# Kernel tuning notes

Hardware: AMD Instinct MI355X
Metric: run time of the kernel (lower is better)

Reference implementation:

```python
import jax, jax.numpy as jnp
import numpy as np

WS = (2, 7, 7)   # window size (d, h, w)
NH = 4           # num heads
EPS = 1e-5       # LayerNorm eps (torch default)


def _rel_index():
    wd, wh, ww = WS
    coords = np.stack(np.meshgrid(np.arange(wd), np.arange(wh), np.arange(ww), indexing='ij'))  # (3,wd,wh,ww)
    cf = coords.reshape(3, -1)                      # (3, N)
    rel = cf[:, :, None] - cf[:, None, :]           # (3, N, N)
    rel = rel.transpose(1, 2, 0).astype(np.int64)   # (N, N, 3)
    rel[..., 0] += wd - 1
    rel[..., 1] += wh - 1
    rel[..., 2] += ww - 1
    rel[..., 0] *= (2 * wh - 1) * (2 * ww - 1)
    rel[..., 1] *= (2 * ww - 1)
    return jnp.asarray(rel.sum(-1), dtype=jnp.int32)  # (N, N)


def setup_inputs() -> dict:
    key = jax.random.key(0)
    ks = jax.random.split(key, 6)
    C, CH = 128, 512
    TBL = (2 * WS[0] - 1) * (2 * WS[1] - 1) * (2 * WS[2] - 1)  # 507
    rn = lambda k, s, sc=0.02: jax.random.normal(k, s, jnp.float32) * sc
    return {
        'x': jax.random.normal(ks[0], (2, 8, 56, 56, C), jnp.float32),
        'norm1_w': jnp.ones((C,), jnp.float32), 'norm1_b': jnp.zeros((C,), jnp.float32),
        'qkv_w': rn(ks[1], (3 * C, C)), 'qkv_b': jnp.zeros((3 * C,), jnp.float32),
        'bias_table': rn(ks[2], (TBL, NH)),
        'proj_w': rn(ks[3], (C, C)), 'proj_b': jnp.zeros((C,), jnp.float32),
        'norm2_w': jnp.ones((C,), jnp.float32), 'norm2_b': jnp.zeros((C,), jnp.float32),
        'fc1_w': rn(ks[4], (CH, C)), 'fc1_b': jnp.zeros((CH,), jnp.float32),
        'fc2_w': rn(ks[5], (C, CH)), 'fc2_b': jnp.zeros((C,), jnp.float32),
        'rel_index': _rel_index(),
    }


def _layernorm(x, w, b):
    m = jnp.mean(x, axis=-1, keepdims=True)
    v = jnp.mean(jnp.square(x - m), axis=-1, keepdims=True)
    return (x - m) * jax.lax.rsqrt(v + EPS) * w + b


def reference(x, norm1_w, norm1_b, qkv_w, qkv_b, bias_table, proj_w, proj_b,
              norm2_w, norm2_b, fc1_w, fc1_b, fc2_w, fc2_b, rel_index):
    B, D, H, W, C = x.shape
    wd, wh, ww = WS
    N = wd * wh * ww
    hd = C // NH

    shortcut = x
    xn = _layernorm(x, norm1_w, norm1_b)
    # window partition: (B,D,H,W,C) -> (B*nW, N, C)
    xw = xn.reshape(B, D // wd, wd, H // wh, wh, W // ww, ww, C)
    xw = xw.transpose(0, 1, 3, 5, 2, 4, 6, 7).reshape(-1, N, C)
    B_ = xw.shape[0]

    qkv = (xw @ qkv_w.T + qkv_b).reshape(B_, N, 3, NH, hd).transpose(2, 0, 3, 1, 4)
    q, k, v = qkv[0] * (hd ** -0.5), qkv[1], qkv[2]   # (B_, NH, N, hd)
    attn = jnp.einsum('bhnd,bhmd->bhnm', q, k)
    bias = bias_table[rel_index.reshape(-1)].reshape(N, N, NH).transpose(2, 0, 1)  # (NH,N,N)
    attn = jax.nn.softmax(attn + bias[None], axis=-1)
    out = jnp.einsum('bhnm,bhmd->bhnd', attn, v).transpose(0, 2, 1, 3).reshape(B_, N, C)
    out = out @ proj_w.T + proj_b

    # window reverse: (B*nW, N, C) -> (B,D,H,W,C)
    xr = out.reshape(B, D // wd, H // wh, W // ww, wd, wh, ww, C)
    xr = xr.transpose(0, 1, 4, 2, 5, 3, 6, 7).reshape(B, D, H, W, C)

    x = shortcut + xr
    h = _layernorm(x, norm2_w, norm2_b)
    h = jax.nn.gelu(h @ fc1_w.T + fc1_b, approximate=False)  # torch nn.GELU = exact erf
    return x + (h @ fc2_w.T + fc2_b)
```

## Files before the change

### kernel.cpp

```cpp
#include <hip/hip_runtime.h>
#include <hip/hip_bf16.h>

typedef __hip_bfloat16 bf16;
typedef unsigned short u16t;
typedef unsigned int u32t;
typedef __attribute__((ext_vector_type(8))) short bf16x8_t;
typedef __attribute__((ext_vector_type(4))) float f32x4_t;

#define DEVI static __device__ __forceinline__

DEVI float u2f(u32t bits) { union { u32t u; float f; } v; v.u = bits; return v.f; }
DEVI float bflo(u32t u) { return u2f((u & 0xffffu) << 16); }
DEVI float bfhi(u32t u) { return u2f(u & 0xffff0000u); }
DEVI float sh2f(short s) { return u2f(((u32t)(u16t)s) << 16); }
DEVI float bf2f(bf16 h) { return __bfloat162float(h); }
DEVI bf16 f2bf(float f) { return __float2bfloat16(f); }
DEVI u16t f2bfbits(float f) {
  bf16 h = __float2bfloat16(f);
  union { bf16 h; u16t u; } v; v.h = h; return v.u;
}

DEVI void gl_lds16(const void* g, void* l) {
  __builtin_amdgcn_global_load_lds(
      (const __attribute__((address_space(1))) unsigned int*)g,
      (__attribute__((address_space(3))) unsigned int*)l, 16, 0, 0);
}

#define TOK   50176
#define NWIN  512
#define NTOK  98
#define NHEAD 4
#define HDIM  32
#define QSCALE 0.17677669529663687f

__global__ __launch_bounds__(256) void setup_k(
    const float* __restrict__ a, const float* __restrict__ b,
    const float* __restrict__ c, const float* __restrict__ d,
    bf16* __restrict__ o,
    const float* __restrict__ btab, const int* __restrict__ relidx,
    const float* __restrict__ qkv_b, float* __restrict__ BmatT,
    float* __restrict__ bsc) {
  int bx = blockIdx.x;
  if (bx < 768) {
    int i = bx * 256 + threadIdx.x;
    const float* s; int off;
    if (i < 49152)       { s = a; off = 0; }
    else if (i < 65536)  { s = b; off = 49152; }
    else if (i < 131072) { s = c; off = 65536; }
    else                 { s = d; off = 131072; }
    float v = s[i - off];
    if (i < 16384) v *= QSCALE;
    o[i] = f2bf(v);
  } else {
    int idx = (bx - 768) * 256 + threadIdx.x;
    if (idx < NTOK * NTOK) {
      int i = idx / NTOK, j = idx - i * NTOK;
      int r = relidx[idx] * NHEAD;
#pragma unroll
      for (int h = 0; h < NHEAD; h++)
        BmatT[(size_t)(h * NTOK + j) * 112 + i] = btab[r + h];
    }
    if (bx == 768 && threadIdx.x < 384)
      bsc[threadIdx.x] = qkv_b[threadIdx.x] * (threadIdx.x < 128 ? QSCALE : 1.0f);
  }
}

DEVI int winrev(int grow) {
  int nw = grow / NTOK, n = grow - nw * NTOK;
  int wq = nw & 7, hq = (nw >> 3) & 7, dq = (nw >> 6) & 3, bb = nw >> 8;
  int wr = n % 7; int q7 = n / 7; int hr = q7 % 7, dr = q7 / 7;
  return ((bb * 8 + dq * 2 + dr) * 56 + hq * 7 + hr) * 56 + wq * 7 + wr;
}

__global__ __launch_bounds__(512, 4) void qkvln_k(
    const float* __restrict__ x, const float* __restrict__ n1w,
    const float* __restrict__ n1b, const bf16* __restrict__ W,
    const float* __restrict__ bsc, bf16* __restrict__ qkvO)
{
  __shared__ __align__(16) short As[128 * 128];
  __shared__ __align__(16) short Bs[128 * 128];
  const int tid = threadIdx.x;
  const int rowBase = blockIdx.x << 7;
  const int wv = tid >> 6, lane = tid & 63;
  const int q = lane >> 4, r16 = lane & 15;

#pragma unroll
  for (int t = 0; t < 4; t++) {
    int f = tid + (t << 9);
    int row = f >> 4, cs = (f & 15) ^ (row & 15);
    gl_lds16((const u16t*)W + (size_t)row * 128 + (cs << 3), &Bs[f << 3]);
  }

  {
    const int c = lane << 1;
    float lw0 = n1w[c], lw1 = n1w[c + 1];
    float lb0 = n1b[c], lb1 = n1b[c + 1];
#pragma unroll
    for (int rr = 0; rr < 16; rr++) {
      int row = (wv << 4) + rr;
      int tt = winrev(rowBase + row);
      float2 xv = *(const float2*)(x + (size_t)tt * 128 + c);
      float x0 = xv.x, x1 = xv.y;
      float s = x0 + x1, ss = x0 * x0 + x1 * x1;
#pragma unroll
      for (int m = 32; m; m >>= 1) { s += __shfl_xor(s, m); ss += __shfl_xor(ss, m); }
      float mean = s * 0.0078125f;
      float var = ss * 0.0078125f - mean * mean;
      float rstd = rsqrtf(var + 1e-5f);
      float y0 = (x0 - mean) * rstd * lw0 + lb0;
      float y1 = (x1 - mean) * rstd * lw1 + lb1;
      u32t ov = ((u32t)f2bfbits(y1) << 16) | (u32t)f2bfbits(y0);
      int slot = (lane >> 2) ^ (row & 15);
      *(u32t*)&As[(row << 7) + (slot << 3) + ((lane & 3) << 1)] = ov;
    }
  }
  __syncthreads();

#pragma unroll 1
  for (int qt = 0; qt < 3; qt++) {
    if (qt > 0) {
#pragma unroll
      for (int t = 0; t < 4; t++) {
        int f = tid + (t << 9);
        int row = f >> 4, cs = (f & 15) ^ (row & 15);
        gl_lds16((const u16t*)W + (size_t)((qt << 7) + row) * 128 + (cs << 3),
                 &Bs[f << 3]);
      }
      __syncthreads();
    }
    f32x4_t acc[8];
#pragma unroll
    for (int j = 0; j < 8; j++) acc[j] = (f32x4_t){0.f, 0.f, 0.f, 0.f};
#pragma unroll
    for (int ks = 0; ks < 4; ks++) {
      int rowA = (wv << 4) + r16;
      int slotA = ((ks << 2) + q) ^ (rowA & 15);
      bf16x8_t af = *(const bf16x8_t*)&As[(rowA << 7) + (slotA << 3)];
      bf16x8_t bfr[8];
#pragma unroll
      for (int nt = 0; nt < 8; nt++) {
        int row = (nt << 4) + r16;
        int slot = ((ks << 2) + q) ^ (row & 15);
        bfr[nt] = *(const bf16x8_t*)&Bs[(row << 7) + (slot << 3)];
      }
#pragma unroll
      for (int nt = 0; nt < 8; nt++)
        acc[nt] = __builtin_amdgcn_mfma_f32_16x16x32_bf16(af, bfr[nt], acc[nt], 0, 0, 0);
    }
    float bv[8];
#pragma unroll
    for (int nt = 0; nt < 8; nt++) bv[nt] = bsc[(qt << 7) + (nt << 4) + r16];
    __syncthreads();
#pragma unroll
    for (int reg = 0; reg < 4; reg++) {
      int lrow = (wv << 4) + (q << 2) + reg;
#pragma unroll
      for (int nt = 0; nt < 8; nt++)
        Bs[(lrow << 7) + (nt << 4) + r16] = (short)f2bfbits(acc[nt][reg] + bv[nt]);
    }
    __syncthreads();
#pragma unroll
    for (int t = 0; t < 4; t++) {
      int f = tid + (t << 9);
      int row = f >> 4, c8 = (f & 15) << 3;
      size_t ob = (size_t)(rowBase + row) * 384 + (qt << 7) + c8;
      *(uint4*)((u16t*)qkvO + ob) = *(const uint4*)&Bs[(row << 7) + c8];
    }
    if (qt < 2) __syncthreads();
  }
}

__global__ __launch_bounds__(512, 4) void proj_k(
    const bf16* __restrict__ A, const bf16* __restrict__ W,
    const float* __restrict__ bias, const float* __restrict__ resX,
    bf16* __restrict__ outB, bf16* __restrict__ outB2,
    const float* __restrict__ lnw, const float* __restrict__ lnb)
{
  __shared__ __align__(16) short As[128 * 128];
  __shared__ __align__(16) short Bs[128 * 128];
  const int tid = threadIdx.x;
  const int rowBase = blockIdx.x << 7;
  const int wv = tid >> 6, lane = tid & 63;
  const int q = lane >> 4, r16 = lane & 15;
  const int mB = wv << 4;

#pragma unroll
  for (int t = 0; t < 4; t++) {
    int f = tid + (t << 9);
    int row = f >> 4, cs = (f & 15) ^ (row & 15);
    gl_lds16((const u16t*)A + (size_t)(rowBase + row) * 128 + (cs << 3),
             &As[f << 3]);
  }
#pragma unroll
  for (int t = 0; t < 4; t++) {
    int f = tid + (t << 9);
    int row = f >> 4, cs = (f & 15) ^ (row & 15);
    gl_lds16((const u16t*)W + (size_t)row * 128 + (cs << 3), &Bs[f << 3]);
  }
  __syncthreads();

  f32x4_t acc[8];
#pragma unroll
  for (int j = 0; j < 8; j++) acc[j] = (f32x4_t){0.f, 0.f, 0.f, 0.f};
#pragma unroll
  for (int ks = 0; ks < 4; ks++) {
    int rowA = mB + r16;
    int slotA = ((ks << 2) + q) ^ (rowA & 15);
    bf16x8_t af = *(const bf16x8_t*)&As[(rowA << 7) + (slotA << 3)];
    bf16x8_t bfr[8];
#pragma unroll
    for (int nt = 0; nt < 8; nt++) {
      int row = (nt << 4) + r16;
      int slot = ((ks << 2) + q) ^ (row & 15);
      bfr[nt] = *(const bf16x8_t*)&Bs[(row << 7) + (slot << 3)];
    }
#pragma unroll
    for (int nt = 0; nt < 8; nt++)
      acc[nt] = __builtin_amdgcn_mfma_f32_16x16x32_bf16(af, bfr[nt], acc[nt], 0, 0, 0);
  }
  __syncthreads();

  float bv[8];
#pragma unroll
  for (int nt = 0; nt < 8; nt++) bv[nt] = bias[(nt << 4) + r16];

#pragma unroll
  for (int reg = 0; reg < 4; reg++) {
    int lrow = mB + (q << 2) + reg;
#pragma unroll
    for (int nt = 0; nt < 8; nt++)
      As[(lrow << 7) + (nt << 4) + r16] = (short)f2bfbits(acc[nt][reg] + bv[nt]);
  }
  __syncthreads();
#pragma unroll
  for (int t = 0; t < 4; t++) {
    int f = tid + (t << 9);
    int row = f >> 4, c8 = (f & 15) << 3;
    int tt = winrev(rowBase + row);
    size_t ob = (size_t)tt * 128 + c8;
    float4 r0 = *(const float4*)(resX + ob);
    float4 r1 = *(const float4*)(resX + ob + 4);
    short* cs = &As[(row << 7) + c8];
    u16t pk[8];
    pk[0] = f2bfbits(sh2f(cs[0]) + r0.x); pk[1] = f2bfbits(sh2f(cs[1]) + r0.y);
    pk[2] = f2bfbits(sh2f(cs[2]) + r0.z); pk[3] = f2bfbits(sh2f(cs[3]) + r0.w);
    pk[4] = f2bfbits(sh2f(cs[4]) + r1.x); pk[5] = f2bfbits(sh2f(cs[5]) + r1.y);
    pk[6] = f2bfbits(sh2f(cs[6]) + r1.z); pk[7] = f2bfbits(sh2f(cs[7]) + r1.w);
    *(uint4*)((u16t*)outB + ob) = *(const uint4*)pk;
    *(uint4*)cs = *(const uint4*)pk;
  }
  __syncthreads();
  const int c = lane << 1;
  float2 lw = *(const float2*)(lnw + c);
  float2 lb = *(const float2*)(lnb + c);
#pragma unroll 4
  for (int rr = 0; rr < 16; rr++) {
    int row = (wv << 4) + rr;
    u32t u = *(const u32t*)&As[(row << 7) + c];
    float x0 = bflo(u), x1 = bfhi(u);
    float s = x0 + x1, ss = x0 * x0 + x1 * x1;
#pragma unroll
    for (int m = 32; m; m >>= 1) { s += __shfl_xor(s, m); ss += __shfl_xor(ss, m); }
    float mean = s * 0.0078125f;
    float var = ss * 0.0078125f - mean * mean;
    float rstd = rsqrtf(var + 1e-5f);
    float y0 = (x0 - mean) * rstd * lw.x + lb.x;
    float y1 = (x1 - mean) * rstd * lw.y + lb.y;
    int tt = winrev(rowBase + row);
    u32t ov = ((u32t)f2bfbits(y1) << 16) | (u32t)f2bfbits(y0);
    *(u32t*)((u16t*)outB2 + (size_t)tt * 128 + c) = ov;
  }
}

__global__ __launch_bounds__(512, 4) void mlp_fused_k(
    const bf16* __restrict__ Axn, const bf16* __restrict__ F1,
    const bf16* __restrict__ F2, const float* __restrict__ b1,
    const float* __restrict__ b2, const bf16* __restrict__ resB,
    float* __restrict__ out)
{
  __shared__ __align__(16) char smem[81920];
  short* As  = (short*)smem;
  short* F1s = (short*)(smem + 32768);
  short* F2s = (short*)(smem + 49152);
  short* Hs  = (short*)(smem + 65536);
  float* Cf  = (float*)smem;

  const int tid = threadIdx.x;
  const int rowBase = blockIdx.x << 7;
  const int wv = tid >> 6, lane = tid & 63;
  const int q = lane >> 4, r16 = lane & 15;
  const int mB = wv << 4;

#pragma unroll
  for (int t = 0; t < 4; t++) {
    int f = tid + (t << 9);
    int row = f >> 4, cs = (f & 15) ^ (row & 15);
    gl_lds16((const u16t*)Axn + (size_t)(rowBase + row) * 128 + (cs << 3),
             &As[f << 3]);
  }
#pragma unroll
  for (int t = 0; t < 2; t++) {
    int f = tid + (t << 9);
    int row = f >> 4, cs = (f & 15) ^ (row & 15);
    gl_lds16((const u16t*)F1 + (size_t)row * 128 + (cs << 3), &F1s[f << 3]);
  }
#pragma unroll
  for (int t = 0; t < 2; t++) {
    int f = tid + (t << 9);
    int row = f >> 3, cs = (f & 7) ^ (row & 7);
    gl_lds16((const u16t*)F2 + (size_t)row * 512 + (cs << 3), &F2s[f << 3]);
  }
  __syncthreads();

  f32x4_t oacc[8];
#pragma unroll
  for (int j = 0; j < 8; j++) oacc[j] = (f32x4_t){0.f, 0.f, 0.f, 0.f};

#pragma unroll 1
  for (int c = 0; c < 8; c++) {
    if (c > 0) {
#pragma unroll
      for (int t = 0; t < 2; t++) {
        int f = tid + (t << 9);
        int row = f >> 4, cs = (f & 15) ^ (row & 15);
        gl_lds16((const u16t*)F1 + (size_t)(c * 64 + row) * 128 + (cs << 3),
                 &F1s[f << 3]);
      }
#pragma unroll
      for (int t = 0; t < 2; t++) {
        int f = tid + (t << 9);
        int row = f >> 3, cs = (f & 7) ^ (row & 7);
        gl_lds16((const u16t*)F2 + (size_t)row * 512 + c * 64 + (cs << 3),
                 &F2s[f << 3]);
      }
      __syncthreads();
    }

    f32x4_t hacc[4];
#pragma unroll
    for (int j = 0; j < 4; j++) hacc[j] = (f32x4_t){0.f, 0.f, 0.f, 0.f};
#pragma unroll
    for (int ks = 0; ks < 4; ks++) {
      int rowA = mB + r16;
      int slotA = ((ks << 2) + q) ^ (rowA & 15);
      bf16x8_t af = *(const bf16x8_t*)&As[(rowA << 7) + (slotA << 3)];
      bf16x8_t bfr[4];
#pragma unroll
      for (int nt = 0; nt < 4; nt++) {
        int row = (nt << 4) + r16;
        int slot = ((ks << 2) + q) ^ (row & 15);
        bfr[nt] = *(const bf16x8_t*)&F1s[(row << 7) + (slot << 3)];
      }
#pragma unroll
      for (int nt = 0; nt < 4; nt++)
        hacc[nt] = __builtin_amdgcn_mfma_f32_16x16x32_bf16(af, bfr[nt], hacc[nt], 0, 0, 0);
    }

    float bb[4];
#pragma unroll
    for (int nt = 0; nt < 4; nt++) bb[nt] = b1[c * 64 + (nt << 4) + r16];
#pragma unroll
    for (int reg = 0; reg < 4; reg++) {
      int lrow = mB + (q << 2) + reg;
#pragma unroll
      for (int nt = 0; nt < 4; nt++) {
        float v = hacc[nt][reg] + bb[nt];
        v = 0.5f * v * (1.0f + erff(v * 0.70710678118654752f));
        int col = (nt << 4) + r16;
        int sp = (col >> 3) ^ (lrow & 7);
        Hs[(lrow << 6) + (sp << 3) + (col & 7)] = (short)f2bfbits(v);
      }
    }
    __syncthreads();

#pragma unroll
    for (int ks = 0; ks < 2; ks++) {
      int rowA = mB + r16;
      int slotA = ((ks << 2) + q) ^ (rowA & 7);
      bf16x8_t af = *(const bf16x8_t*)&Hs[(rowA << 6) + (slotA << 3)];
      bf16x8_t bfr[8];
#pragma unroll
      for (int nt = 0; nt < 8; nt++) {
        int row = (nt << 4) + r16;
        int slot = ((ks << 2) + q) ^ (row & 7);
        bfr[nt] = *(const bf16x8_t*)&F2s[(row << 6) + (slot << 3)];
      }
#pragma unroll
      for (int nt = 0; nt < 8; nt++)
        oacc[nt] = __builtin_amdgcn_mfma_f32_16x16x32_bf16(af, bfr[nt], oacc[nt], 0, 0, 0);
    }
    __syncthreads();
  }

  float bv[8];
#pragma unroll
  for (int nt = 0; nt < 8; nt++) bv[nt] = b2[(nt << 4) + r16];
#pragma unroll
  for (int reg = 0; reg < 4; reg++) {
    int lrow = mB + (q << 2) + reg;
#pragma unroll
    for (int nt = 0; nt < 8; nt++)
      Cf[lrow * 132 + (nt << 4) + r16] = oacc[nt][reg] + bv[nt];
  }
  __syncthreads();
#pragma unroll
  for (int t = 0; t < 8; t++) {
    int f = tid + (t << 9);
    int row = f >> 5, c4 = (f & 31) << 2;
    size_t ob = (size_t)(rowBase + row) * 128 + c4;
    const u16t* rp = (const u16t*)resB + ob;
    const float* cp = &Cf[row * 132 + c4];
    float4 v;
    v.x = cp[0] + sh2f(rp[0]);
    v.y = cp[1] + sh2f(rp[1]);
    v.z = cp[2] + sh2f(rp[2]);
    v.w = cp[3] + sh2f(rp[3]);
    *(float4*)(out + ob) = v;
  }
}

#define PSTR 136
__global__ __launch_bounds__(256) void attn_mfma_k(
    const bf16* __restrict__ qkv, const float* __restrict__ BmatT,
    bf16* __restrict__ out)
{
  __shared__ short Vt[32 * PSTR];
  __shared__ short Ps[112 * PSTR];
  const int nw = blockIdx.x, h = blockIdx.y;
  const int tid = threadIdx.x;
  const int wv = tid >> 6, lane = tid & 63;
  const int q = lane >> 4, r16 = lane & 15;

  for (int idx = tid; idx < 32 * 38; idx += 256) {
    int d = idx / 38, j = 98 + idx % 38;
    Vt[d * PSTR + j] = 0;
  }
  for (int idx = tid; idx < 112 * 12; idx += 256) {
    int r = idx / 12, c = (idx % 12) << 1;
    *(u32t*)&Ps[r * PSTR + 112 + c] = 0;
  }
  for (int idx = tid; idx < NTOK * 16; idx += 256) {
    int j = idx >> 4, d2 = (idx & 15) << 1;
    u32t uv = *(const u32t*)((const u16t*)qkv +
                             (size_t)(nw * NTOK + j) * 384 + 256 + h * 32 + d2);
    Vt[d2 * PSTR + j] = (short)(uv & 0xffffu);
    Vt[(d2 + 1) * PSTR + j] = (short)(uv >> 16);
  }

  const int mt0 = wv;
  const bool has2 = (wv + 4) < 7;
  const int mt1 = has2 ? wv + 4 : wv;

  int i0 = mt0 * 16 + r16; if (i0 > NTOK - 1) i0 = NTOK - 1;
  int i1 = mt1 * 16 + r16; if (i1 > NTOK - 1) i1 = NTOK - 1;
  bf16x8_t aq0 = *(const bf16x8_t*)((const u16t*)qkv +
      (size_t)(nw * NTOK + i0) * 384 + h * 32 + (q << 3));
  bf16x8_t aq1 = *(const bf16x8_t*)((const u16t*)qkv +
      (size_t)(nw * NTOK + i1) * 384 + h * 32 + (q << 3));

  f32x4_t sc[2][7];
#pragma unroll
  for (int nt = 0; nt < 7; nt++) {
    int j = (nt << 4) + r16; if (j > NTOK - 1) j = NTOK - 1;
    const float* bRow = &BmatT[(size_t)(h * NTOK + j) * 112];
    bf16x8_t bk = *(const bf16x8_t*)((const u16t*)qkv +
        (size_t)(nw * NTOK + j) * 384 + 128 + h * 32 + (q << 3));
    f32x4_t b0 = *(const f32x4_t*)&bRow[mt0 * 16 + (q << 2)];
    f32x4_t b1 = *(const f32x4_t*)&bRow[mt1 * 16 + (q << 2)];
    sc[0][nt] = __builtin_amdgcn_mfma_f32_16x16x32_bf16(aq0, bk, b0, 0, 0, 0);
    sc[1][nt] = __builtin_amdgcn_mfma_f32_16x16x32_bf16(aq1, bk, b1, 0, 0, 0);
  }

#pragma unroll
  for (int sel = 0; sel < 2; sel++) {
    if (sel == 1 && !has2) break;
    int mtile = sel ? mt1 : mt0;
    int ibase = mtile * 16 + (q << 2);
    float s[4][7];
#pragma unroll
    for (int nt = 0; nt < 7; nt++) {
      int j = (nt << 4) + r16;
#pragma unroll
      for (int reg = 0; reg < 4; reg++) {
        int i = ibase + reg;
        s[reg][nt] = (i < NTOK && j < NTOK) ? sc[sel][nt][reg] : -1.0e30f;
      }
    }
#pragma unroll
    for (int reg = 0; reg < 4; reg++) {
      float m = -3.0e38f;
#pragma unroll
      for (int nt = 0; nt < 7; nt++) m = fmaxf(m, s[reg][nt]);
#pragma unroll
      for (int d = 8; d; d >>= 1) m = fmaxf(m, __shfl_xor(m, d));
      float sum = 0.f;
#pragma unroll
      for (int nt = 0; nt < 7; nt++) { s[reg][nt] = __expf(s[reg][nt] - m); sum += s[reg][nt]; }
#pragma unroll
      for (int d = 8; d; d >>= 1) sum += __shfl_xor(sum, d);
      float inv = 1.f / sum;
#pragma unroll
      for (int nt = 0; nt < 7; nt++)
        Ps[(ibase + reg) * PSTR + (nt << 4) + r16] =
            (short)f2bfbits(s[reg][nt] * inv);
    }
  }

  __syncthreads();

#pragma unroll
  for (int sel = 0; sel < 2; sel++) {
    if (sel == 1 && !has2) break;
    int mtile = sel ? mt1 : mt0;
    f32x4_t o0 = {0.f, 0.f, 0.f, 0.f}, o1 = {0.f, 0.f, 0.f, 0.f};
#pragma unroll
    for (int kt = 0; kt < 4; kt++) {
      bf16x8_t ap = *(const bf16x8_t*)&Ps[(mtile * 16 + r16) * PSTR + (kt << 5) + (q << 3)];
      bf16x8_t bv0 = *(const bf16x8_t*)&Vt[r16 * PSTR + (kt << 5) + (q << 3)];
      bf16x8_t bv1 = *(const bf16x8_t*)&Vt[(16 + r16) * PSTR + (kt << 5) + (q << 3)];
      o0 = __builtin_amdgcn_mfma_f32_16x16x32_bf16(ap, bv0, o0, 0, 0, 0);
      o1 = __builtin_amdgcn_mfma_f32_16x16x32_bf16(ap, bv1, o1, 0, 0, 0);
    }
#pragma unroll
    for (int reg = 0; reg < 4; reg++) {
      int i = mtile * 16 + (q << 2) + reg;
      if (i < NTOK) {
        size_t ob = (size_t)(nw * NTOK + i) * 128 + h * 32;
        out[ob + r16] = f2bf(o0[reg]);
        out[ob + 16 + r16] = f2bf(o1[reg]);
      }
    }
  }
}

extern "C" void kernel_launch(void* const* d_in, const int* in_sizes, int n_in,
                              void* d_out, int out_size, void* d_ws, size_t ws_size,
                              hipStream_t stream) {
  const float* x      = (const float*)d_in[0];
  const float* n1w    = (const float*)d_in[1];
  const float* n1b    = (const float*)d_in[2];
  const float* qkv_w  = (const float*)d_in[3];
  const float* qkv_b  = (const float*)d_in[4];
  const float* btab   = (const float*)d_in[5];
  const float* proj_w = (const float*)d_in[6];
  const float* proj_b = (const float*)d_in[7];
  const float* n2w    = (const float*)d_in[8];
  const float* n2b    = (const float*)d_in[9];
  const float* fc1_w  = (const float*)d_in[10];
  const float* fc1_b  = (const float*)d_in[11];
  const float* fc2_w  = (const float*)d_in[12];
  const float* fc2_b  = (const float*)d_in[13];
  const int*   relidx = (const int*)d_in[14];

  const size_t Asz = (size_t)TOK * 128 * 2;
  char* ws = (char*)d_ws;
  bf16* wbf   = (bf16*)ws;
  bf16* qkvw16  = wbf;
  bf16* projw16 = wbf + 49152;
  bf16* fc1w16  = wbf + 65536;
  bf16* fc2w16  = wbf + 131072;
  float* BmatT = (float*)(ws + 393216);
  float* bsc   = (float*)(ws + 393216 + 175616);
  char* R = ws + (1 << 20);
  bf16* attn  = (bf16*)d_out;
  bf16* qkv   = (bf16*)R;
  bf16* x2    = (bf16*)R;
  bf16* xn2   = (bf16*)(R + Asz);
  float* out  = (float*)d_out;

  setup_k<<<806, 256, 0, stream>>>(qkv_w, proj_w, fc1_w, fc2_w, wbf,
                                   btab, relidx, qkv_b, BmatT, bsc);
  qkvln_k<<<TOK / 128, 512, 0, stream>>>(x, n1w, n1b, qkvw16, bsc, qkv);
  attn_mfma_k<<<dim3(NWIN, NHEAD), 256, 0, stream>>>(qkv, BmatT, attn);
  proj_k<<<TOK / 128, 512, 0, stream>>>(
      attn, projw16, proj_b, x, x2, xn2, n2w, n2b);
  mlp_fused_k<<<TOK / 128, 512, 0, stream>>>(
      xn2, fc1w16, fc2w16, fc1_b, fc2_b, x2, out);
}
```

Measured before the change: 203.9 us.

## Double-buffer MLP weight chunks and halve chunk width in fused MLP kernel

```diff
diff --git a/kernel.cpp b/kernel.cpp
--- a/kernel.cpp
+++ b/kernel.cpp
@@ -278,12 +278,10 @@
     const float* __restrict__ b2, const bf16* __restrict__ resB,
     float* __restrict__ out)
 {
-  __shared__ __align__(16) char smem[81920];
-  short* As  = (short*)smem;
-  short* F1s = (short*)(smem + 32768);
-  short* F2s = (short*)(smem + 49152);
-  short* Hs  = (short*)(smem + 65536);
-  float* Cf  = (float*)smem;
+  __shared__ __align__(16) char smem[73728];
+  short* As = (short*)smem;
+  short* Hs = (short*)(smem + 65536);
+  float* Cf = (float*)smem;
 
   const int tid = threadIdx.x;
   const int rowBase = blockIdx.x << 7;
@@ -298,17 +296,13 @@
     gl_lds16((const u16t*)Axn + (size_t)(rowBase + row) * 128 + (cs << 3),
              &As[f << 3]);
   }
-#pragma unroll
-  for (int t = 0; t < 2; t++) {
-    int f = tid + (t << 9);
-    int row = f >> 4, cs = (f & 15) ^ (row & 15);
-    gl_lds16((const u16t*)F1 + (size_t)row * 128 + (cs << 3), &F1s[f << 3]);
-  }
-#pragma unroll
-  for (int t = 0; t < 2; t++) {
-    int f = tid + (t << 9);
-    int row = f >> 3, cs = (f & 7) ^ (row & 7);
-    gl_lds16((const u16t*)F2 + (size_t)row * 512 + (cs << 3), &F2s[f << 3]);
+  {
+    int row = tid >> 4, cs = (tid & 15) ^ (row & 15);
+    gl_lds16((const u16t*)F1 + (size_t)row * 128 + (cs << 3),
+             (short*)(smem + 32768) + (tid << 3));
+    int row2 = tid >> 2, cs2 = (tid & 3) ^ (row2 & 3);
+    gl_lds16((const u16t*)F2 + (size_t)row2 * 512 + (cs2 << 3),
+             (short*)(smem + 49152) + (tid << 3));
   }
   __syncthreads();
 
@@ -317,73 +311,64 @@
   for (int j = 0; j < 8; j++) oacc[j] = (f32x4_t){0.f, 0.f, 0.f, 0.f};
 
 #pragma unroll 1
-  for (int c = 0; c < 8; c++) {
-    if (c > 0) {
-#pragma unroll
-      for (int t = 0; t < 2; t++) {
-        int f = tid + (t << 9);
-        int row = f >> 4, cs = (f & 15) ^ (row & 15);
-        gl_lds16((const u16t*)F1 + (size_t)(c * 64 + row) * 128 + (cs << 3),
-                 &F1s[f << 3]);
-      }
-#pragma unroll
-      for (int t = 0; t < 2; t++) {
-        int f = tid + (t << 9);
-        int row = f >> 3, cs = (f & 7) ^ (row & 7);
-        gl_lds16((const u16t*)F2 + (size_t)row * 512 + c * 64 + (cs << 3),
-                 &F2s[f << 3]);
-      }
-      __syncthreads();
-    }
-
-    f32x4_t hacc[4];
-#pragma unroll
-    for (int j = 0; j < 4; j++) hacc[j] = (f32x4_t){0.f, 0.f, 0.f, 0.f};
+  for (int c = 0; c < 16; c++) {
+    const int p = c & 1;
+    short* F1s = (short*)(smem + 32768 + (p << 13));
+    short* F2s = (short*)(smem + 49152 + (p << 13));
+    if (c < 15) {
+      short* F1n = (short*)(smem + 32768 + ((p ^ 1) << 13));
+      short* F2n = (short*)(smem + 49152 + ((p ^ 1) << 13));
+      int row = tid >> 4, cs = (tid & 15) ^ (row & 15);
+      gl_lds16((const u16t*)F1 + (size_t)((c + 1) * 32 + row) * 128 + (cs << 3),
+               F1n + (tid << 3));
+      int row2 = tid >> 2, cs2 = (tid & 3) ^ (row2 & 3);
+      gl_lds16((const u16t*)F2 + (size_t)row2 * 512 + (c + 1) * 32 + (cs2 << 3),
+               F2n + (tid << 3));
+    }
+
+    f32x4_t hacc[2];
+#pragma unroll
+    for (int j = 0; j < 2; j++) hacc[j] = (f32x4_t){0.f, 0.f, 0.f, 0.f};
 #pragma unroll
     for (int ks = 0; ks < 4; ks++) {
       int rowA = mB + r16;
       int slotA = ((ks << 2) + q) ^ (rowA & 15);
       bf16x8_t af = *(const bf16x8_t*)&As[(rowA << 7) + (slotA << 3)];
-      bf16x8_t bfr[4];
-#pragma unroll
-      for (int nt = 0; nt < 4; nt++) {
+      bf16x8_t bfr[2];
+#pragma unroll
+      for (int nt = 0; nt < 2; nt++) {
         int row = (nt << 4) + r16;
         int slot = ((ks << 2) + q) ^ (row & 15);
         bfr[nt] = *(const bf16x8_t*)&F1s[(row << 7) + (slot << 3)];
       }
 #pragma unroll
-      for (int nt = 0; nt < 4; nt++)
+      for (int nt = 0; nt < 2; nt++)
         hacc[nt] = __builtin_amdgcn_mfma_f32_16x16x32_bf16(af, bfr[nt], hacc[nt], 0, 0, 0);
     }
 
-    float bb[4];
-#pragma unroll
-    for (int nt = 0; nt < 4; nt++) bb[nt] = b1[c * 64 + (nt << 4) + r16];
 #pragma unroll
     for (int reg = 0; reg < 4; reg++) {
       int lrow = mB + (q << 2) + reg;
 #pragma unroll
-      for (int nt = 0; nt < 4; nt++) {
-        float v = hacc[nt][reg] + bb[nt];
+      for (int nt = 0; nt < 2; nt++) {
+        float v = hacc[nt][reg] + b1[c * 32 + (nt << 4) + r16];
         v = 0.5f * v * (1.0f + erff(v * 0.70710678118654752f));
         int col = (nt << 4) + r16;
-        int sp = (col >> 3) ^ (lrow & 7);
-        Hs[(lrow << 6) + (sp << 3) + (col & 7)] = (short)f2bfbits(v);
-      }
-    }
-    __syncthreads();
-
-#pragma unroll
-    for (int ks = 0; ks < 2; ks++) {
+        int sp = (col >> 3) ^ (lrow & 3);
+        Hs[(lrow << 5) + (sp << 3) + (col & 7)] = (short)f2bfbits(v);
+      }
+    }
+
+    {
       int rowA = mB + r16;
-      int slotA = ((ks << 2) + q) ^ (rowA & 7);
-      bf16x8_t af = *(const bf16x8_t*)&Hs[(rowA << 6) + (slotA << 3)];
+      int slotA = q ^ (rowA & 3);
+      bf16x8_t af = *(const bf16x8_t*)&Hs[(rowA << 5) + (slotA << 3)];
       bf16x8_t bfr[8];
 #pragma unroll
       for (int nt = 0; nt < 8; nt++) {
         int row = (nt << 4) + r16;
-        int slot = ((ks << 2) + q) ^ (row & 7);
-        bfr[nt] = *(const bf16x8_t*)&F2s[(row << 6) + (slot << 3)];
+        int slot = q ^ (row & 3);
+        bfr[nt] = *(const bf16x8_t*)&F2s[(row << 5) + (slot << 3)];
       }
 #pragma unroll
       for (int nt = 0; nt < 8; nt++)
```

Result: no change. 205.8 us (+0.9%).
